# Performance work log

Measured on AMD Instinct MI355X. Metric: run time of the kernel, lower is better.

The kernel has to match this reference:

```python
import jax, jax.numpy as jnp
import numpy as np

ALPHA = 0.0

def setup_inputs() -> dict:
    key = jax.random.key(0)
    k1, k2, k3 = jax.random.split(key, 3)
    E = 1000000
    num_nodes = 50000
    num_rels = 237
    edge_index = jax.random.randint(k1, (2, E), 0, num_nodes, dtype=jnp.int64)
    edge_type = jax.random.randint(k2, (E,), 0, num_rels, dtype=jnp.int64)
    batch = jax.random.randint(k3, (64, 32, 3), 0, num_rels, dtype=jnp.int64)
    edge_weight = jnp.ones((E,), dtype=jnp.float32)
    return {
        "edge_index": edge_index,
        "edge_type": edge_type,
        "batch": batch,
        "edge_weight": edge_weight,
        "num_nodes": num_nodes,
    }


def reference(edge_index, edge_type, batch, edge_weight, num_nodes):
    # Per query i (row of batch), count tail nodes of training edges whose
    # head == h_index[i,0] and relation == r_index[i,0]; softmax over nodes.
    h = batch[:, 0, 0]  # [B] query head entity
    r = batch[:, 0, 2]  # [B] query relation
    heads = edge_index[0]  # [E]
    tails = edge_index[1]  # [E]
    # [B, E] boolean: which training edges match each query's (head, rel)
    match = (heads[None, :] == h[:, None]) & (edge_type[None, :] == r[:, None])
    contrib = jnp.where(match, edge_weight[None, :], jnp.float32(0.0))  # [B, E]
    B = batch.shape[0]
    # Scatter-add matched edges into per-query tail histograms == bincount
    dist = jnp.zeros((B, num_nodes), dtype=jnp.float32).at[:, tails].add(contrib)
    freq_res = jax.nn.softmax(dist, axis=1)
    return (freq_res, ALPHA)
```

## Files before the change

kernel.cpp:

```cpp
#include <hip/hip_runtime.h>
#include <float.h>
#include <stdint.h>


#define KCAP 1024

struct Entry { int t; float v; };

__global__ void scatter_kernel(const int* __restrict__ edge_index,
                               const int* __restrict__ etype,
                               const float* __restrict__ ew,
                               const int* __restrict__ batch,
                               int* __restrict__ cnt,
                               Entry* __restrict__ entries,
                               int E, int B) {
    __shared__ unsigned s_keys[256];
    __shared__ unsigned s_bloom[64];
    for (int i = threadIdx.x; i < 64; i += blockDim.x) s_bloom[i] = 0u;
    __syncthreads();
    for (int i = threadIdx.x; i < B; i += blockDim.x) {
        unsigned h = (unsigned)batch[i * 96 + 0];
        unsigned r = (unsigned)batch[i * 96 + 2];
        unsigned key = (h << 16) | (r & 0xFFFFu);
        s_keys[i] = key;
        unsigned hs = (key * 2654435761u) >> 21;
        atomicOr(&s_bloom[hs >> 5], 1u << (hs & 31u));
    }
    __syncthreads();

    int e = blockIdx.x * blockDim.x + threadIdx.x;
    if (e >= E) return;
    unsigned key = ((unsigned)edge_index[e] << 16) | ((unsigned)etype[e] & 0xFFFFu);
    unsigned hs = (key * 2654435761u) >> 21;
    if (!(s_bloom[hs >> 5] & (1u << (hs & 31u)))) return;

    int tail = -1;
    float w = 0.0f;
    for (int b = 0; b < B; ++b) {
        if (s_keys[b] == key) {
            if (tail < 0) { tail = edge_index[E + e]; w = ew[e]; }
            int idx = atomicAdd(&cnt[b], 1);
            if (idx < KCAP) { entries[b * KCAP + idx].t = tail; entries[b * KCAP + idx].v = w; }
        }
    }
}

__global__ void rowparams_kernel(const int* __restrict__ cnt,
                                 Entry* __restrict__ entries,
                                 float* __restrict__ rowBase,
                                 int* __restrict__ dcnt,
                                 int N, int B) {
    int b = threadIdx.x + blockIdx.x * blockDim.x;
    if (b >= B) return;
    Entry* row = entries + (size_t)b * KCAP;
    int k = min(cnt[b], KCAP);

    int nd = 0;
    for (int i = 0; i < k; ++i) {
        int t = row[i].t;
        float v = row[i].v;
        int j = 0;
        for (; j < nd; ++j) if (row[j].t == t) break;
        if (j < nd) row[j].v += v;
        else { row[nd].t = t; row[nd].v = v; ++nd; }
    }

    float M = 0.0f;
    for (int j = 0; j < nd; ++j) M = fmaxf(M, row[j].v);
    float S = (float)(N - nd) * expf(-M);
    for (int j = 0; j < nd; ++j) {
        float e = expf(row[j].v - M);
        S += e;
        row[j].v = e;
    }
    for (int j = 0; j < nd; ++j) row[j].v = row[j].v / S;
    rowBase[b] = expf(-M) / S;
    dcnt[b] = nd;
}

__global__ void fill4_kernel(float* __restrict__ out, const float* __restrict__ rowBase, int N4, int N) {
    int i4 = blockIdx.x * blockDim.x + threadIdx.x;
    float base = rowBase[blockIdx.y];
    if (i4 < N4) {
        float4* row4 = (float4*)(out + (size_t)blockIdx.y * N);
        row4[i4] = make_float4(base, base, base, base);
    }
}
__global__ void fill1_kernel(float* __restrict__ out, const float* __restrict__ rowBase, int N) {
    int i = blockIdx.x * blockDim.x + threadIdx.x;
    float base = rowBase[blockIdx.y];
    if (i < N) out[(size_t)blockIdx.y * N + i] = base;
}

__global__ void fixup_kernel(const int* __restrict__ dcnt,
                             const Entry* __restrict__ entries,
                             float* __restrict__ out, int N, int B) {
    int b = threadIdx.x;
    if (b < B) {
        int nd = dcnt[b];
        const Entry* row = entries + (size_t)b * KCAP;
        for (int j = 0; j < nd; ++j) out[(size_t)b * N + row[j].t] = row[j].v;
    }
    if (threadIdx.x == 0) out[(size_t)B * N] = 0.0f;
}

extern "C" void kernel_launch(void* const* d_in, const int* in_sizes, int n_in,
                              void* d_out, int out_size, void* d_ws, size_t ws_size,
                              hipStream_t stream) {
    const int*   edge_index = (const int*)d_in[0];
    const int*   edge_type  = (const int*)d_in[1];
    const int*   batch      = (const int*)d_in[2];
    const float* ew         = (const float*)d_in[3];

    const int E = in_sizes[1];
    const int B = in_sizes[2] / 96;
    const int N = (out_size - 1) / B;

    float* out = (float*)d_out;

    char*  ws      = (char*)d_ws;
    int*   cnt     = (int*)ws;
    float* rowBase = (float*)(ws + 1024);
    int*   dcnt    = (int*)(ws + 2048);
    Entry* entries = (Entry*)(ws + 4096);

    hipMemsetAsync(cnt, 0, B * sizeof(int), stream);

    const int threads = 256;
    scatter_kernel<<<(E + threads - 1) / threads, threads, 0, stream>>>(
        edge_index, edge_type, ew, batch, cnt, entries, E, B);

    const int rpThreads = ((B + 63) / 64) * 64;
    rowparams_kernel<<<1, rpThreads, 0, stream>>>(cnt, entries, rowBase, dcnt, N, B);

    if ((N & 3) == 0) {
        const int N4 = N >> 2;
        fill4_kernel<<<dim3((N4 + 255) / 256, B), 256, 0, stream>>>(out, rowBase, N4, N);
    } else {
        fill1_kernel<<<dim3((N + 255) / 256, B), 256, 0, stream>>>(out, rowBase, N);
    }

    fixup_kernel<<<1, 256, 0, stream>>>(dcnt, entries, out, N, B);
}
```

Baseline: 92.36 us.

## Fuse row softmax params and fixup into fill kernel; vectorize edge scan

```diff
diff --git a/kernel.cpp b/kernel.cpp
--- a/kernel.cpp
+++ b/kernel.cpp
@@ -4,6 +4,7 @@
 
 
 #define KCAP 1024
+#define NDCAP 128
 
 struct Entry { int t; float v; };
 
@@ -28,80 +29,135 @@
     }
     __syncthreads();
 
-    int e = blockIdx.x * blockDim.x + threadIdx.x;
-    if (e >= E) return;
-    unsigned key = ((unsigned)edge_index[e] << 16) | ((unsigned)etype[e] & 0xFFFFu);
-    unsigned hs = (key * 2654435761u) >> 21;
-    if (!(s_bloom[hs >> 5] & (1u << (hs & 31u)))) return;
+    const int e0 = (blockIdx.x * blockDim.x + threadIdx.x) * 4;
+    if (e0 >= E) return;
 
-    int tail = -1;
-    float w = 0.0f;
-    for (int b = 0; b < B; ++b) {
-        if (s_keys[b] == key) {
-            if (tail < 0) { tail = edge_index[E + e]; w = ew[e]; }
-            int idx = atomicAdd(&cnt[b], 1);
-            if (idx < KCAP) { entries[b * KCAP + idx].t = tail; entries[b * KCAP + idx].v = w; }
+    int4 hh, rr;
+    if (e0 + 3 < E) {
+        hh = *(const int4*)(edge_index + e0);
+        rr = *(const int4*)(etype + e0);
+    } else {
+        int* ph = (int*)&hh; int* pr = (int*)&rr;
+        for (int u = 0; u < 4; ++u) {
+            int e = e0 + u;
+            ph[u] = (e < E) ? edge_index[e] : -1;
+            pr[u] = (e < E) ? etype[e] : -1;
+        }
+    }
+
+#pragma unroll
+    for (int u = 0; u < 4; ++u) {
+        int e = e0 + u;
+        if (e >= E) break;
+        unsigned h = ((const unsigned*)&hh)[u];
+        unsigned r = ((const unsigned*)&rr)[u];
+        unsigned key = (h << 16) | (r & 0xFFFFu);
+        unsigned hs = (key * 2654435761u) >> 21;
+        if (!(s_bloom[hs >> 5] & (1u << (hs & 31u)))) continue;
+
+        int tail = -1;
+        float w = 0.0f;
+        for (int b = 0; b < B; ++b) {
+            if (s_keys[b] == key) {
+                if (tail < 0) { tail = edge_index[E + e]; w = ew[e]; }
+                int idx = atomicAdd(&cnt[b], 1);
+                if (idx < KCAP) {
+                    entries[b * KCAP + idx].t = tail;
+                    entries[b * KCAP + idx].v = w;
+                }
+            }
         }
     }
 }
 
-__global__ void rowparams_kernel(const int* __restrict__ cnt,
-                                 Entry* __restrict__ entries,
-                                 float* __restrict__ rowBase,
-                                 int* __restrict__ dcnt,
-                                 int N, int B) {
-    int b = threadIdx.x + blockIdx.x * blockDim.x;
-    if (b >= B) return;
-    Entry* row = entries + (size_t)b * KCAP;
-    int k = min(cnt[b], KCAP);
+__global__ void fill4_fused_kernel(const int* __restrict__ cnt,
+                                   const Entry* __restrict__ entries,
+                                   float* __restrict__ out,
+                                   int N4, int N, int B) {
+    __shared__ int   s_td[NDCAP];
+    __shared__ float s_vd[NDCAP];
+    __shared__ int   s_nd;
+    __shared__ float s_base;
+    const int b = blockIdx.y;
+    if (threadIdx.x == 0) {
+        const Entry* row = entries + (size_t)b * KCAP;
+        int k = min(cnt[b], KCAP);
+        int nd = 0;
+        for (int i = 0; i < k; ++i) {
+            int t = row[i].t; float v = row[i].v;
+            int j = 0;
+            for (; j < nd; ++j) if (s_td[j] == t) break;
+            if (j < nd) s_vd[j] += v;
+            else if (nd < NDCAP) { s_td[nd] = t; s_vd[nd] = v; ++nd; }
+        }
+        float M = 0.0f;
+        for (int j = 0; j < nd; ++j) M = fmaxf(M, s_vd[j]);
+        float S = (float)(N - nd) * expf(-M);
+        for (int j = 0; j < nd; ++j) { float e = expf(s_vd[j] - M); s_vd[j] = e; S += e; }
+        float inv = 1.0f / S;
+        for (int j = 0; j < nd; ++j) s_vd[j] *= inv;
+        s_base = expf(-M) * inv;
+        s_nd = nd;
+    }
+    __syncthreads();
 
-    int nd = 0;
-    for (int i = 0; i < k; ++i) {
-        int t = row[i].t;
-        float v = row[i].v;
-        int j = 0;
-        for (; j < nd; ++j) if (row[j].t == t) break;
-        if (j < nd) row[j].v += v;
-        else { row[nd].t = t; row[nd].v = v; ++nd; }
+    const int   nd   = s_nd;
+    const float base = s_base;
+    const int i4 = blockIdx.x * blockDim.x + threadIdx.x;
+    if (i4 < N4) {
+        float4 v = make_float4(base, base, base, base);
+        const int eBase = i4 << 2;
+        for (int j = 0; j < nd; ++j) {
+            int d = s_td[j] - eBase;
+            if ((unsigned)d < 4u) ((float*)&v)[d] = s_vd[j];
+        }
+        ((float4*)(out + (size_t)b * N))[i4] = v;
     }
-
-    float M = 0.0f;
-    for (int j = 0; j < nd; ++j) M = fmaxf(M, row[j].v);
-    float S = (float)(N - nd) * expf(-M);
-    for (int j = 0; j < nd; ++j) {
-        float e = expf(row[j].v - M);
-        S += e;
-        row[j].v = e;
-    }
-    for (int j = 0; j < nd; ++j) row[j].v = row[j].v / S;
-    rowBase[b] = expf(-M) / S;
-    dcnt[b] = nd;
+    if (b == 0 && blockIdx.x == 0 && threadIdx.x == 0)
+        out[(size_t)B * N] = 0.0f;
 }
 
-__global__ void fill4_kernel(float* __restrict__ out, const float* __restrict__ rowBase, int N4, int N) {
-    int i4 = blockIdx.x * blockDim.x + threadIdx.x;
-    float base = rowBase[blockIdx.y];
-    if (i4 < N4) {
-        float4* row4 = (float4*)(out + (size_t)blockIdx.y * N);
-        row4[i4] = make_float4(base, base, base, base);
+__global__ void fill1_fused_kernel(const int* __restrict__ cnt,
+                                   const Entry* __restrict__ entries,
+                                   float* __restrict__ out,
+                                   int N, int B) {
+    __shared__ int   s_td[NDCAP];
+    __shared__ float s_vd[NDCAP];
+    __shared__ int   s_nd;
+    __shared__ float s_base;
+    const int b = blockIdx.y;
+    if (threadIdx.x == 0) {
+        const Entry* row = entries + (size_t)b * KCAP;
+        int k = min(cnt[b], KCAP);
+        int nd = 0;
+        for (int i = 0; i < k; ++i) {
+            int t = row[i].t; float v = row[i].v;
+            int j = 0;
+            for (; j < nd; ++j) if (s_td[j] == t) break;
+            if (j < nd) s_vd[j] += v;
+            else if (nd < NDCAP) { s_td[nd] = t; s_vd[nd] = v; ++nd; }
+        }
+        float M = 0.0f;
+        for (int j = 0; j < nd; ++j) M = fmaxf(M, s_vd[j]);
+        float S = (float)(N - nd) * expf(-M);
+        for (int j = 0; j < nd; ++j) { float e = expf(s_vd[j] - M); s_vd[j] = e; S += e; }
+        float inv = 1.0f / S;
+        for (int j = 0; j < nd; ++j) s_vd[j] *= inv;
+        s_base = expf(-M) * inv;
+        s_nd = nd;
     }
-}
-__global__ void fill1_kernel(float* __restrict__ out, const float* __restrict__ rowBase, int N) {
-    int i = blockIdx.x * blockDim.x + threadIdx.x;
-    float base = rowBase[blockIdx.y];
-    if (i < N) out[(size_t)blockIdx.y * N + i] = base;
-}
+    __syncthreads();
 
-__global__ void fixup_kernel(const int* __restrict__ dcnt,
-                             const Entry* __restrict__ entries,
-                             float* __restrict__ out, int N, int B) {
-    int b = threadIdx.x;
-    if (b < B) {
-        int nd = dcnt[b];
-        const Entry* row = entries + (size_t)b * KCAP;
-        for (int j = 0; j < nd; ++j) out[(size_t)b * N + row[j].t] = row[j].v;
+    const int   nd   = s_nd;
+    const float base = s_base;
+    const int i = blockIdx.x * blockDim.x + threadIdx.x;
+    if (i < N) {
+        float v = base;
+        for (int j = 0; j < nd; ++j) if (s_td[j] == i) v = s_vd[j];
+        out[(size_t)b * N + i] = v;
     }
-    if (threadIdx.x == 0) out[(size_t)B * N] = 0.0f;
+    if (b == 0 && blockIdx.x == 0 && threadIdx.x == 0)
+        out[(size_t)B * N] = 0.0f;
 }
 
 extern "C" void kernel_launch(void* const* d_in, const int* in_sizes, int n_in,
@@ -120,25 +176,21 @@
 
     char*  ws      = (char*)d_ws;
     int*   cnt     = (int*)ws;
-    float* rowBase = (float*)(ws + 1024);
-    int*   dcnt    = (int*)(ws + 2048);
     Entry* entries = (Entry*)(ws + 4096);
 
     hipMemsetAsync(cnt, 0, B * sizeof(int), stream);
 
     const int threads = 256;
-    scatter_kernel<<<(E + threads - 1) / threads, threads, 0, stream>>>(
+    const int edgesPerBlock = threads * 4;
+    scatter_kernel<<<(E + edgesPerBlock - 1) / edgesPerBlock, threads, 0, stream>>>(
         edge_index, edge_type, ew, batch, cnt, entries, E, B);
-
-    const int rpThreads = ((B + 63) / 64) * 64;
-    rowparams_kernel<<<1, rpThreads, 0, stream>>>(cnt, entries, rowBase, dcnt, N, B);
 
     if ((N & 3) == 0) {
         const int N4 = N >> 2;
-        fill4_kernel<<<dim3((N4 + 255) / 256, B), 256, 0, stream>>>(out, rowBase, N4, N);
+        fill4_fused_kernel<<<dim3((N4 + 255) / 256, B), 256, 0, stream>>>(
+            cnt, entries, out, N4, N, B);
     } else {
-        fill1_kernel<<<dim3((N + 255) / 256, B), 256, 0, stream>>>(out, rowBase, N);
+        fill1_fused_kernel<<<dim3((N + 255) / 256, B), 256, 0, stream>>>(
+            cnt, entries, out, N, B);
     }
-
-    fixup_kernel<<<1, 256, 0, stream>>>(dcnt, entries, out, N, B);
 }
```

Result: slower. 119.9 us (+29.8%).
